# Performance work log

Hardware: AMD Instinct MI355X
Metric: run time of the kernel (lower is better)

## Reference

```python
import math
import jax, jax.numpy as jnp
import numpy as np

B, S, D, H = 2, 512, 1024, 8
DK = D // H
NSEP = 4


def setup_inputs() -> dict:
    key = jax.random.key(0)
    ks = jax.random.split(key, 16)
    inp = {
        'query': jax.random.normal(ks[0], (B, S, D), jnp.float32),
        'key': jax.random.normal(ks[1], (B, S, D), jnp.float32),
        'value': jax.random.normal(ks[2], (B, S, D), jnp.float32),
        'relation_k': jax.random.normal(ks[3], (B, S, S, DK), jnp.float32),
        'relation_v': jax.random.normal(ks[4], (B, S, S, DK), jnp.float32),
        'mask': jnp.ones((B, S, S), jnp.int32),
        'sep_id': jnp.sort(jax.random.randint(ks[5], (NSEP,), 0, S)),
        'history_reg': jax.random.uniform(ks[6], (1, NSEP), jnp.float32),
        'Wq': jax.random.normal(ks[7], (D, D), jnp.float32) / math.sqrt(D),
        'bq': jnp.zeros((D,), jnp.float32),
        'Wk': jax.random.normal(ks[8], (D, D), jnp.float32) / math.sqrt(D),
        'bk': jnp.zeros((D,), jnp.float32),
        'Wv': jax.random.normal(ks[9], (D, D), jnp.float32) / math.sqrt(D),
        'bv': jnp.zeros((D,), jnp.float32),
        'Wo': jax.random.normal(ks[10], (D, D), jnp.float32) / math.sqrt(D),
        'bo': jnp.zeros((D,), jnp.float32),
        'history_weights': jax.random.normal(ks[11], (H, DK), jnp.float32) / math.sqrt(DK),
    }
    return inp


def reference(query, key, value, relation_k, relation_v, mask, sep_id, history_reg,
              Wq, bq, Wk, bk, Wv, bv, Wo, bo, history_weights):
    b, s, d = query.shape
    h = history_weights.shape[0]
    dk = d // h
    scale = 1.0 / math.sqrt(dk)

    def proj(x, W, bb):
        return (x @ W.T + bb).reshape(b, s, h, dk).transpose(0, 2, 1, 3)  # [B,H,S,dk]

    q = proj(query, Wq, bq)
    k = proj(key, Wk, bk)
    v = proj(value, Wv, bv)

    # relation-aware logits: QK^T + Q.relation_k^T, scaled
    scores = (jnp.einsum('bhqd,bhkd->bhqk', q, k)
              + jnp.einsum('bhqd,bqkd->bhqk', q, relation_k)) * scale
    scores = jnp.where(mask[:, None, :, :] == 0, -1000000000.0, scores)

    # per-segment history reweighting
    sep_sel = q[:, :, sep_id, :]                                   # [B,H,n,dk]
    sep_pool = jnp.einsum('bhnd,hd->bhn', sep_sel, history_weights)
    sep_pred = jax.nn.softmax(sep_pool, axis=-1)                   # [B,H,n]

    pos = jnp.arange(s)
    ind = (pos[None, :] >= sep_id[:, None]).astype(scores.dtype)   # [n,S]
    g = jnp.einsum('bhn,np->bhp', sep_pred, ind)                   # cum weight per position
    minrc = jnp.minimum(pos[:, None], pos[None, :])                # [S,S]
    factor = g[:, :, minrc]                                        # [B,H,S,S]
    scores = scores * factor

    # losses
    loss = jnp.mean(1.0 - jnp.max(jnp.abs(sep_pred), axis=-1))
    log_pred = jnp.log(sep_pred).reshape(-1, sep_pred.shape[-1])
    tgt = jnp.broadcast_to(history_reg, log_pred.shape)
    loss = loss + jnp.mean(tgt * (jnp.log(tgt) - log_pred))

    p = jax.nn.softmax(scores, axis=-1)  # dropout is identity at eval
    x = (jnp.einsum('bhqk,bhkd->bhqd', p, v)
         + jnp.einsum('bhqk,bqkd->bhqd', p, relation_v))
    x = x.transpose(0, 2, 1, 3).reshape(b, s, d)
    out = x @ Wo.T + bo
    return out, loss
```

## Files before the change

### kernel.cpp

```cpp
#include <hip/hip_runtime.h>

static constexpr float SCALE = 0.08838834764831845f;

typedef __bf16 bf16;
typedef __bf16 bf16x8 __attribute__((ext_vector_type(8)));
typedef float  f32x4  __attribute__((ext_vector_type(4)));

#define MFMA16(a, b, c) __builtin_amdgcn_mfma_f32_16x16x32_bf16((a), (b), (c), 0, 0, 0)

__device__ inline bf16x8 cvt8(const float4& x, const float4& y) {
  bf16x8 r;
  r[0] = (bf16)x.x; r[1] = (bf16)x.y; r[2] = (bf16)x.z; r[3] = (bf16)x.w;
  r[4] = (bf16)y.x; r[5] = (bf16)y.y; r[6] = (bf16)y.z; r[7] = (bf16)y.w;
  return r;
}

__global__ __launch_bounds__(256)
void cvt_bf16(const float* __restrict__ s0, const float* __restrict__ s1,
              const float* __restrict__ s2, const float* __restrict__ s3,
              const float* __restrict__ s4, const float* __restrict__ s5,
              const float* __restrict__ s6,
              bf16* __restrict__ d0, bf16* __restrict__ d1,
              bf16* __restrict__ d2, bf16* __restrict__ d3,
              bf16* __restrict__ d4, bf16* __restrict__ d5,
              bf16* __restrict__ d6)
{
  const int sel = blockIdx.y;
  const float* src = sel == 0 ? s0 : sel == 1 ? s1 : sel == 2 ? s2 :
                     sel == 3 ? s3 : sel == 4 ? s4 : sel == 5 ? s5 : s6;
  bf16* dst = sel == 0 ? d0 : sel == 1 ? d1 : sel == 2 ? d2 :
              sel == 3 ? d3 : sel == 4 ? d4 : sel == 5 ? d5 : d6;
  const size_t idx = ((size_t)blockIdx.x * 256 + threadIdx.x) * 8;
  const float4 a = *(const float4*)(src + idx);
  const float4 b = *(const float4*)(src + idx + 4);
  *(bf16x8*)(dst + idx) = cvt8(a, b);
}

__global__ __launch_bounds__(256)
void proj3_mfma2(const bf16* __restrict__ Aq, const bf16* __restrict__ Ak,
                 const bf16* __restrict__ Av,
                 const bf16* __restrict__ Wq, const bf16* __restrict__ Wk,
                 const bf16* __restrict__ Wv,
                 const float* __restrict__ bq, const float* __restrict__ bk,
                 const float* __restrict__ bv,
                 float* __restrict__ qf, bf16* __restrict__ q16,
                 bf16* __restrict__ k16, bf16* __restrict__ vt16)
{
  const int sel = blockIdx.y;
  const bf16* A     = sel == 0 ? Aq : (sel == 1 ? Ak : Av);
  const bf16* W     = sel == 0 ? Wq : (sel == 1 ? Wk : Wv);
  const float* bias = sel == 0 ? bq : (sel == 1 ? bk : bv);

  __shared__ bf16 As[64][72];
  __shared__ bf16 Bs[64][72];
  const int t = threadIdx.x;
  const int m0 = (blockIdx.x >> 4) << 6;
  const int n0 = (blockIdx.x & 15) << 6;
  const int wave = t >> 6, lane = t & 63;
  const int wr = wave >> 1, wc = wave & 1;
  const int srow = t >> 2, skc = (t & 3) << 4;
  const bf16* Ap = A + (size_t)(m0 + srow) * 1024 + skc;
  const bf16* Wp = W + (size_t)(n0 + srow) * 1024 + skc;
  const int fr = lane & 15, kb = (lane >> 4) << 3;
  f32x4 acc[2][2];
#pragma unroll
  for (int i = 0; i < 2; ++i)
#pragma unroll
    for (int j = 0; j < 2; ++j) acc[i][j] = (f32x4){0.f, 0.f, 0.f, 0.f};

  uint4 a0 = *(const uint4*)Ap, a1 = *(const uint4*)(Ap + 8);
  uint4 b0 = *(const uint4*)Wp, b1 = *(const uint4*)(Wp + 8);
  uint4 a0n, a1n, b0n, b1n;
  for (int k0 = 0; k0 < 1024; k0 += 64) {
    __syncthreads();
    *(uint4*)&As[srow][skc]     = a0; *(uint4*)&As[srow][skc + 8] = a1;
    *(uint4*)&Bs[srow][skc]     = b0; *(uint4*)&Bs[srow][skc + 8] = b1;
    __syncthreads();
    if (k0 + 64 < 1024) {
      a0n = *(const uint4*)(Ap + k0 + 64); a1n = *(const uint4*)(Ap + k0 + 72);
      b0n = *(const uint4*)(Wp + k0 + 64); b1n = *(const uint4*)(Wp + k0 + 72);
    }
#pragma unroll
    for (int ks = 0; ks < 2; ++ks) {
      bf16x8 af[2], bff[2];
#pragma unroll
      for (int f = 0; f < 2; ++f) {
        af[f]  = *(const bf16x8*)&As[wr * 32 + f * 16 + fr][ks * 32 + kb];
        bff[f] = *(const bf16x8*)&Bs[wc * 32 + f * 16 + fr][ks * 32 + kb];
      }
#pragma unroll
      for (int i = 0; i < 2; ++i)
#pragma unroll
        for (int j = 0; j < 2; ++j)
          acc[i][j] = MFMA16(af[i], bff[j], acc[i][j]);
    }
    a0 = a0n; a1 = a1n; b0 = b0n; b1 = b1n;
  }
  const int lrow = (lane >> 4) << 2, lcol = lane & 15;
#pragma unroll
  for (int i = 0; i < 2; ++i) {
#pragma unroll
    for (int j = 0; j < 2; ++j) {
      const int n = n0 + wc * 32 + j * 16 + lcol;
      const float bvl = bias[n];
#pragma unroll
      for (int r = 0; r < 4; ++r) {
        const int m = m0 + wr * 32 + i * 16 + lrow + r;
        const float val = acc[i][j][r] + bvl;
        const int b = m >> 9, ii = m & 511, h = n >> 7, dk = n & 127;
        if (sel == 2) {
          vt16[(((size_t)(b * 8 + h) * 128) + dk) * 512 + ii] = (bf16)val;
        } else {
          const size_t idx = (((size_t)(b * 8 + h) * 512) + ii) * 128 + dk;
          if (sel == 0) { qf[idx] = val; q16[idx] = (bf16)val; }
          else          { k16[idx] = (bf16)val; }
        }
      }
    }
  }
}

__global__ __launch_bounds__(256)
void qs_fat(const bf16* __restrict__ Q, const bf16* __restrict__ Kb,
            float* __restrict__ scores,
            const float* __restrict__ qf, const float* __restrict__ hw,
            const int* __restrict__ sep_id, const float* __restrict__ hreg,
            float* __restrict__ g, float* __restrict__ loss_out)
{
  __shared__ bf16 As[64][72];
  __shared__ bf16 Bs[64][72];
  __shared__ float pool[16][4];
  __shared__ float spred[16][4];
  __shared__ float lbuf[16];
  __shared__ int sids[4];
  const int t = threadIdx.x;

  if (blockIdx.x >= 1024) {
    if (t < 4) sids[t] = sep_id[t];
    __syncthreads();
    {
      const int dot = t >> 2, sub = t & 3;
      const int bh = dot >> 2, n = dot & 3;
      const int b = bh >> 3, h = bh & 7;
      const int row = sids[n];
      const float* qp = qf + (((size_t)(b * 8 + h) * 512) + row) * 128 + sub * 32;
      const float* wp = hw + h * 128 + sub * 32;
      float s = 0.f;
#pragma unroll
      for (int dd = 0; dd < 32; ++dd) s = fmaf(qp[dd], wp[dd], s);
      s += __shfl_xor(s, 1);
      s += __shfl_xor(s, 2);
      if (sub == 0) pool[bh][n] = s;
    }
    __syncthreads();
    if (t < 16) {
      float pv[4];
#pragma unroll
      for (int n = 0; n < 4; ++n) pv[n] = pool[t][n];
      float mx = fmaxf(fmaxf(pv[0], pv[1]), fmaxf(pv[2], pv[3]));
      float sum = 0.f;
#pragma unroll
      for (int n = 0; n < 4; ++n) { pv[n] = expf(pv[n] - mx); sum += pv[n]; }
      const float inv = 1.f / sum;
      float maxp = 0.f, l2 = 0.f;
#pragma unroll
      for (int n = 0; n < 4; ++n) {
        const float pr = pv[n] * inv;
        spred[t][n] = pr;
        maxp = fmaxf(maxp, pr);
        const float tg = hreg[n];
        l2 += tg * (logf(tg) - logf(pr));
      }
      lbuf[t] = (1.f - maxp) / 16.f + l2 / 64.f;
    }
    __syncthreads();
    if (t == 0) {
      float L = 0.f;
#pragma unroll
      for (int r = 0; r < 16; ++r) L += lbuf[r];
      loss_out[0] = L;
    }
    for (int idx = t; idx < 16 * 512; idx += 256) {
      const int bh = idx >> 9, pp = idx & 511;
      float gg = 0.f;
#pragma unroll
      for (int n = 0; n < 4; ++n)
        gg += spred[bh][n] * (pp >= sids[n] ? 1.f : 0.f);
      g[idx] = gg;
    }
    return;
  }

  const int bh = blockIdx.x >> 6, tile = blockIdx.x & 63;
  const bf16* A = Q  + (size_t)bh * (512 * 128);
  const bf16* B = Kb + (size_t)bh * (512 * 128);
  float* C = scores + (size_t)bh * (512 * 512);
  const int m0 = (tile >> 3) << 6, n0 = (tile & 7) << 6;
  const int wave = t >> 6, lane = t & 63;
  const int wr = wave >> 1, wc = wave & 1;
  const int srow = t >> 2, skc = (t & 3) << 4;
  const int fr = lane & 15, kb = (lane >> 4) << 3;
  f32x4 acc[2][2];
#pragma unroll
  for (int i = 0; i < 2; ++i)
#pragma unroll
    for (int j = 0; j < 2; ++j) acc[i][j] = (f32x4){0.f, 0.f, 0.f, 0.f};

  const bf16* ap = A + (size_t)(m0 + srow) * 128 + skc;
  const bf16* bp = B + (size_t)(n0 + srow) * 128 + skc;
  uint4 a0 = *(const uint4*)ap, a1 = *(const uint4*)(ap + 8);
  uint4 b0 = *(const uint4*)bp, b1 = *(const uint4*)(bp + 8);
  for (int k0 = 0; k0 < 128; k0 += 64) {
    __syncthreads();
    *(uint4*)&As[srow][skc]     = a0; *(uint4*)&As[srow][skc + 8] = a1;
    *(uint4*)&Bs[srow][skc]     = b0; *(uint4*)&Bs[srow][skc + 8] = b1;
    __syncthreads();
    if (k0 == 0) {
      a0 = *(const uint4*)(ap + 64); a1 = *(const uint4*)(ap + 72);
      b0 = *(const uint4*)(bp + 64); b1 = *(const uint4*)(bp + 72);
    }
#pragma unroll
    for (int ks = 0; ks < 2; ++ks) {
      bf16x8 af[2], bff[2];
#pragma unroll
      for (int f = 0; f < 2; ++f) {
        af[f]  = *(const bf16x8*)&As[wr * 32 + f * 16 + fr][ks * 32 + kb];
        bff[f] = *(const bf16x8*)&Bs[wc * 32 + f * 16 + fr][ks * 32 + kb];
      }
#pragma unroll
      for (int i = 0; i < 2; ++i)
#pragma unroll
        for (int j = 0; j < 2; ++j)
          acc[i][j] = MFMA16(af[i], bff[j], acc[i][j]);
    }
  }
  const int lrow = (lane >> 4) << 2, lcol = lane & 15;
#pragma unroll
  for (int i = 0; i < 2; ++i)
#pragma unroll
    for (int j = 0; j < 2; ++j)
#pragma unroll
      for (int r = 0; r < 4; ++r) {
        const int m = m0 + wr * 32 + i * 16 + lrow + r;
        const int n = n0 + wc * 32 + j * 16 + lcol;
        C[(size_t)m * 512 + n] = acc[i][j][r];
      }
}

__global__ __launch_bounds__(256)
void relk_sm(const bf16* __restrict__ q16, const float* __restrict__ rk,
             const float* __restrict__ sc, const int* __restrict__ mask,
             const float* __restrict__ g, bf16* __restrict__ pb)
{
  const int bi = blockIdx.x, b = bi >> 9, i = bi & 511;
  __shared__ float rel_[8 * 516];
  const int t = threadIdx.x;
  const int w = t >> 6, lane = t & 63;
  const int fr = lane & 15, fg = lane >> 4;

  bf16x8 bq[4];
#pragma unroll
  for (int kt = 0; kt < 4; ++kt) {
    if (fr < 8) {
      bq[kt] = *(const bf16x8*)&q16[(((size_t)(b * 8 + fr) * 512) + i) * 128
                                    + kt * 32 + fg * 8];
    } else {
#pragma unroll
      for (int e = 0; e < 8; ++e) bq[kt][e] = (bf16)0.f;
    }
  }

  const float* rkb = rk + (size_t)bi * 512 * 128;
  for (int c = 0; c < 8; ++c) {
    const int jb = c * 64 + w * 16;
    const float* rp = rkb + (size_t)(jb + fr) * 128 + fg * 8;
    float4 a[8];
#pragma unroll
    for (int kt = 0; kt < 4; ++kt) {
      a[kt * 2]     = *(const float4*)(rp + kt * 32);
      a[kt * 2 + 1] = *(const float4*)(rp + kt * 32 + 4);
    }
    f32x4 acc = (f32x4){0.f, 0.f, 0.f, 0.f};
#pragma unroll
    for (int kt = 0; kt < 4; ++kt)
      acc = MFMA16(cvt8(a[kt * 2], a[kt * 2 + 1]), bq[kt], acc);
    if (fr < 8) {
#pragma unroll
      for (int r = 0; r < 4; ++r)
        rel_[fr * 516 + jb + fg * 4 + r] = acc[r];
    }
  }
  __syncthreads();

  const int h = t >> 5, ln = t & 31;
  const float* scrow = sc + (((size_t)(b * 8 + h) * 512) + i) * 512;
  const int* mrow = mask + ((size_t)(b * 512 + i)) * 512;
  const float* grow = g + (b * 8 + h) * 512;
  const float gi = grow[i];
  float s[16];
  float mx = -3.402823466e+38f;
#pragma unroll
  for (int k = 0; k < 16; ++k) {
    const int j = ln + (k << 5);
    float sv = (scrow[j] + rel_[h * 516 + j]) * SCALE;
    if (mrow[j] == 0) sv = -1.0e9f;
    const float fac = (j >= i) ? gi : grow[j];
    sv *= fac;
    s[k] = sv;
    mx = fmaxf(mx, sv);
  }
#pragma unroll
  for (int off = 16; off > 0; off >>= 1) mx = fmaxf(mx, __shfl_xor(mx, off));
  float sum = 0.f;
#pragma unroll
  for (int k = 0; k < 16; ++k) { const float e = __expf(s[k] - mx); s[k] = e; sum += e; }
#pragma unroll
  for (int off = 16; off > 0; off >>= 1) sum += __shfl_xor(sum, off);
  const float inv = 1.f / sum;
  bf16* prow = pb + (((size_t)(b * 8 + h) * 512) + i) * 512;
#pragma unroll
  for (int k = 0; k < 16; ++k) {
    const int j = ln + (k << 5);
    prow[j] = (bf16)(s[k] * inv);
  }
}

__global__ __launch_bounds__(256)
void relv_fat(const bf16* __restrict__ P, const bf16* __restrict__ VT,
              const float* __restrict__ rvg,
              float* __restrict__ xb2, float* __restrict__ xa)
{
  __shared__ __align__(16) char smem_raw[26032];
  const int t = threadIdx.x;

  if (blockIdx.x < 256) {
    bf16 (*As)[72] = (bf16(*)[72])&smem_raw[0];
    bf16 (*Bs)[72] = (bf16(*)[72])&smem_raw[9216];
    const int bh = blockIdx.x >> 4, tile = blockIdx.x & 15;
    const int b = bh >> 3, h = bh & 7;
    const bf16* A = P  + (size_t)bh * (512 * 512);
    const bf16* B = VT + (size_t)bh * (128 * 512);
    float* C = xb2 + (size_t)b * (512 * 1024) + h * 128;
    const int m0 = (tile >> 1) << 6, n0 = (tile & 1) << 6;
    const int wave = t >> 6, lane = t & 63;
    const int wr = wave >> 1, wc = wave & 1;
    const int srow = t >> 2, skc = (t & 3) << 4;
    const int fr = lane & 15, kb = (lane >> 4) << 3;
    f32x4 acc[2][2];
#pragma unroll
    for (int i = 0; i < 2; ++i)
#pragma unroll
      for (int j = 0; j < 2; ++j) acc[i][j] = (f32x4){0.f, 0.f, 0.f, 0.f};

    const bf16* ap = A + (size_t)(m0 + srow) * 512 + skc;
    const bf16* bp = B + (size_t)(n0 + srow) * 512 + skc;
    uint4 a0 = *(const uint4*)ap, a1 = *(const uint4*)(ap + 8);
    uint4 b0 = *(const uint4*)bp, b1 = *(const uint4*)(bp + 8);
    for (int k0 = 0; k0 < 512; k0 += 64) {
      __syncthreads();
      *(uint4*)&As[srow][skc]     = a0; *(uint4*)&As[srow][skc + 8] = a1;
      *(uint4*)&Bs[srow][skc]     = b0; *(uint4*)&Bs[srow][skc + 8] = b1;
      __syncthreads();
      if (k0 + 64 < 512) {
        a0 = *(const uint4*)(ap + k0 + 64); a1 = *(const uint4*)(ap + k0 + 72);
        b0 = *(const uint4*)(bp + k0 + 64); b1 = *(const uint4*)(bp + k0 + 72);
      }
#pragma unroll
      for (int ks = 0; ks < 2; ++ks) {
        bf16x8 af[2], bff[2];
#pragma unroll
        for (int f = 0; f < 2; ++f) {
          af[f]  = *(const bf16x8*)&As[wr * 32 + f * 16 + fr][ks * 32 + kb];
          bff[f] = *(const bf16x8*)&Bs[wc * 32 + f * 16 + fr][ks * 32 + kb];
        }
#pragma unroll
        for (int i = 0; i < 2; ++i)
#pragma unroll
          for (int j = 0; j < 2; ++j)
            acc[i][j] = MFMA16(af[i], bff[j], acc[i][j]);
      }
    }
    const int lrow = (lane >> 4) << 2, lcol = lane & 15;
#pragma unroll
    for (int i = 0; i < 2; ++i)
#pragma unroll
      for (int j = 0; j < 2; ++j)
#pragma unroll
        for (int r = 0; r < 4; ++r) {
          const int m = m0 + wr * 32 + i * 16 + lrow + r;
          const int n = n0 + wc * 32 + j * 16 + lcol;
          C[(size_t)m * 1024 + n] = acc[i][j][r];
        }
    return;
  }

  const int bi = blockIdx.x - 256, b = bi >> 9, i = bi & 511;
  bf16* p_lds = (bf16*)&smem_raw[0];
  bf16* rvT   = (bf16*)&smem_raw[9648];
  const int w = t >> 6, lane = t & 63;
  const int fr = lane & 15, fg = lane >> 4;

  {
    const int h = t >> 5, j0 = (t & 31) << 4;
    const bf16* src = P + (((size_t)(b * 8 + h) * 512) + i) * 512 + j0;
    const uint4 v0 = *(const uint4*)src;
    const uint4 v1 = *(const uint4*)(src + 8);
    *(uint4*)&p_lds[h * 536 + j0]     = v0;
    *(uint4*)&p_lds[h * 536 + j0 + 8] = v1;
  }

  const int arow = (fr < 8) ? fr : 8;
  const int ct0 = w * 2, ct1 = w * 2 + 1;
  f32x4 acc0 = (f32x4){0.f, 0.f, 0.f, 0.f};
  f32x4 acc1 = (f32x4){0.f, 0.f, 0.f, 0.f};

  for (int ch = 0; ch < 8; ++ch) {
    const int j0 = ch * 64;
    __syncthreads();
    {
      const int jj = t >> 5, d0 = (t & 31) << 2;
#pragma unroll
      for (int ps = 0; ps < 8; ++ps) {
        const int j = jj + ps * 8;
        const float4 rr = *(const float4*)&rvg[((size_t)bi * 512 + j0 + j) * 128 + d0];
        const float vr[4] = {rr.x, rr.y, rr.z, rr.w};
#pragma unroll
        for (int r = 0; r < 4; ++r) {
          const int d = d0 + r;
          const int blk = ((j >> 3) + (d >> 2)) & 7;
          rvT[d * 64 + blk * 8 + (j & 7)] = (bf16)vr[r];
        }
      }
    }
    __syncthreads();
#pragma unroll
    for (int kl = 0; kl < 2; ++kl) {
      const int jsub = kl * 32 + fg * 8;
      const bf16x8 af = *(const bf16x8*)&p_lds[arow * 536 + j0 + jsub];
      {
        const int d = ct0 * 16 + fr;
        const int blk = ((jsub >> 3) + (d >> 2)) & 7;
        const bf16x8 bf_ = *(const bf16x8*)&rvT[d * 64 + blk * 8];
        acc0 = MFMA16(af, bf_, acc0);
      }
      {
        const int d = ct1 * 16 + fr;
        const int blk = ((jsub >> 3) + (d >> 2)) & 7;
        const bf16x8 bf_ = *(const bf16x8*)&rvT[d * 64 + blk * 8];
        acc1 = MFMA16(af, bf_, acc1);
      }
    }
  }

  if (fg < 2) {
    float* xrow = xa + ((size_t)(b * 512 + i)) * 1024;
#pragma unroll
    for (int r = 0; r < 4; ++r) {
      const int h = fg * 4 + r;
      xrow[h * 128 + ct0 * 16 + fr] = acc0[r];
      xrow[h * 128 + ct1 * 16 + fr] = acc1[r];
    }
  }
}

__global__ __launch_bounds__(256)
void proj_out2(const float* __restrict__ A, const float* __restrict__ A2,
               const bf16* __restrict__ W16,
               const float* __restrict__ bias, float* __restrict__ Cf)
{
  __shared__ bf16 As[64][72];
  __shared__ bf16 Bs[64][72];
  const int t = threadIdx.x;
  const int m0 = (blockIdx.x >> 4) << 6;
  const int n0 = (blockIdx.x & 15) << 6;
  const int wave = t >> 6, lane = t & 63;
  const int wr = wave >> 1, wc = wave & 1;
  const int srow = t >> 2, skc = (t & 3) << 4;
  const float* Ap  = A   + (size_t)(m0 + srow) * 1024 + skc;
  const float* A2p = A2  + (size_t)(m0 + srow) * 1024 + skc;
  const bf16*  Wp  = W16 + (size_t)(n0 + srow) * 1024 + skc;
  const int fr = lane & 15, kb = (lane >> 4) << 3;
  f32x4 acc[2][2];
#pragma unroll
  for (int i = 0; i < 2; ++i)
#pragma unroll
    for (int j = 0; j < 2; ++j) acc[i][j] = (f32x4){0.f, 0.f, 0.f, 0.f};

  float4 a4[4], a4n[4];
  uint4 b0 = *(const uint4*)Wp, b1 = *(const uint4*)(Wp + 8);
  uint4 b0n, b1n;
#pragma unroll
  for (int u = 0; u < 4; ++u) {
    const float4 x1 = *(const float4*)(Ap + u * 4);
    const float4 x2 = *(const float4*)(A2p + u * 4);
    a4[u] = make_float4(x1.x + x2.x, x1.y + x2.y, x1.z + x2.z, x1.w + x2.w);
  }
  for (int k0 = 0; k0 < 1024; k0 += 64) {
    __syncthreads();
    *(bf16x8*)&As[srow][skc]     = cvt8(a4[0], a4[1]);
    *(bf16x8*)&As[srow][skc + 8] = cvt8(a4[2], a4[3]);
    *(uint4*)&Bs[srow][skc]      = b0;
    *(uint4*)&Bs[srow][skc + 8]  = b1;
    __syncthreads();
    if (k0 + 64 < 1024) {
#pragma unroll
      for (int u = 0; u < 4; ++u) {
        const float4 x1 = *(const float4*)(Ap + k0 + 64 + u * 4);
        const float4 x2 = *(const float4*)(A2p + k0 + 64 + u * 4);
        a4n[u] = make_float4(x1.x + x2.x, x1.y + x2.y, x1.z + x2.z, x1.w + x2.w);
      }
      b0n = *(const uint4*)(Wp + k0 + 64);
      b1n = *(const uint4*)(Wp + k0 + 72);
    }
#pragma unroll
    for (int ks = 0; ks < 2; ++ks) {
      bf16x8 af[2], bff[2];
#pragma unroll
      for (int f = 0; f < 2; ++f) {
        af[f]  = *(const bf16x8*)&As[wr * 32 + f * 16 + fr][ks * 32 + kb];
        bff[f] = *(const bf16x8*)&Bs[wc * 32 + f * 16 + fr][ks * 32 + kb];
      }
#pragma unroll
      for (int i = 0; i < 2; ++i)
#pragma unroll
        for (int j = 0; j < 2; ++j)
          acc[i][j] = MFMA16(af[i], bff[j], acc[i][j]);
    }
#pragma unroll
    for (int u = 0; u < 4; ++u) a4[u] = a4n[u];
    b0 = b0n; b1 = b1n;
  }
  const int lrow = (lane >> 4) << 2, lcol = lane & 15;
#pragma unroll
  for (int i = 0; i < 2; ++i) {
#pragma unroll
    for (int j = 0; j < 2; ++j) {
      const int n = n0 + wc * 32 + j * 16 + lcol;
      const float bvl = bias[n];
#pragma unroll
      for (int r = 0; r < 4; ++r) {
        const int m = m0 + wr * 32 + i * 16 + lrow + r;
        Cf[(size_t)m * 1024 + n] = acc[i][j][r] + bvl;
      }
    }
  }
}

extern "C" void kernel_launch(void* const* d_in, const int* in_sizes, int n_in,
                              void* d_out, int out_size, void* d_ws, size_t ws_size,
                              hipStream_t stream)
{
  const float* query = (const float*)d_in[0];
  const float* key   = (const float*)d_in[1];
  const float* value = (const float*)d_in[2];
  const float* rk    = (const float*)d_in[3];
  const float* rv    = (const float*)d_in[4];
  const int*   mask  = (const int*)d_in[5];
  const int*   sep   = (const int*)d_in[6];
  const float* hreg  = (const float*)d_in[7];
  const float* Wq    = (const float*)d_in[8];
  const float* bq    = (const float*)d_in[9];
  const float* Wk    = (const float*)d_in[10];
  const float* bk    = (const float*)d_in[11];
  const float* Wv    = (const float*)d_in[12];
  const float* bv    = (const float*)d_in[13];
  const float* Wo    = (const float*)d_in[14];
  const float* bo    = (const float*)d_in[15];
  const float* hw    = (const float*)d_in[16];
  float* out = (float*)d_out;

  float* ws  = (float*)d_ws;
  float* qb  = ws;
  float* sc  = qb + 1048576;
  float* xa  = sc + 4194304;
  float* xb2 = xa + 1048576;
  float* gb  = xb2 + 1048576;
  bf16* qb16 = (bf16*)(gb + 8192);
  bf16* kb16 = qb16 + 1048576;
  bf16* vt16 = kb16 + 1048576;
  bf16* pb16 = vt16 + 1048576;
  bf16* qA16 = pb16;
  bf16* kA16 = qA16 + 1048576;
  bf16* vA16 = kA16 + 1048576;
  bf16* Wq16 = vA16 + 1048576;
  bf16* Wk16 = pb16 + 4194304;
  bf16* Wv16 = Wk16 + 1048576;
  bf16* Wo16 = Wv16 + 1048576;

  cvt_bf16<<<dim3(512, 7), 256, 0, stream>>>(query, key, value, Wq, Wk, Wv, Wo,
                                             qA16, kA16, vA16, Wq16, Wk16, Wv16,
                                             Wo16);
  proj3_mfma2<<<dim3(256, 3), 256, 0, stream>>>(qA16, kA16, vA16,
                                                Wq16, Wk16, Wv16, bq, bk, bv,
                                                qb, qb16, kb16, vt16);
  qs_fat<<<dim3(1025), 256, 0, stream>>>(qb16, kb16, sc,
                                         qb, hw, sep, hreg, gb, out + 1048576);
  relk_sm<<<dim3(1024), 256, 0, stream>>>(qb16, rk, sc, mask, gb, pb16);
  relv_fat<<<dim3(1280), 256, 0, stream>>>(pb16, vt16, rv, xb2, xa);
  proj_out2<<<dim3(256), 256, 0, stream>>>(xa, xb2, Wo16, bo, out);
}
```

Measured before the change: 176.5 us.

## Double-buffer GEMM LDS tiles and stream relation_v directly from global into MFMA operands

The projection GEMMs now ping-pong between two LDS buffers, which removes one of the two barriers per k-step. The relation_v path in relv_fat no longer stages a transposed bf16 copy in LDS with a barrier per chunk. Instead each lane gathers strided fp32 values straight from global memory, converts them, and feeds them as the A operand with P as the B operand, which swaps the output layout. This drops LDS traffic and syncs, but the relation_v loads become scattered scalar reads that coalesce poorly and may raise global memory transactions.

```diff
diff --git a/kernel.cpp b/kernel.cpp
--- a/kernel.cpp
+++ b/kernel.cpp
@@ -51,8 +51,8 @@
   const bf16* W     = sel == 0 ? Wq : (sel == 1 ? Wk : Wv);
   const float* bias = sel == 0 ? bq : (sel == 1 ? bk : bv);
 
-  __shared__ bf16 As[64][72];
-  __shared__ bf16 Bs[64][72];
+  __shared__ bf16 As[2][64][72];
+  __shared__ bf16 Bs[2][64][72];
   const int t = threadIdx.x;
   const int m0 = (blockIdx.x >> 4) << 6;
   const int n0 = (blockIdx.x & 15) << 6;
@@ -72,21 +72,21 @@
   uint4 b0 = *(const uint4*)Wp, b1 = *(const uint4*)(Wp + 8);
   uint4 a0n, a1n, b0n, b1n;
   for (int k0 = 0; k0 < 1024; k0 += 64) {
-    __syncthreads();
-    *(uint4*)&As[srow][skc]     = a0; *(uint4*)&As[srow][skc + 8] = a1;
-    *(uint4*)&Bs[srow][skc]     = b0; *(uint4*)&Bs[srow][skc + 8] = b1;
-    __syncthreads();
+    const int buf = (k0 >> 6) & 1;
+    *(uint4*)&As[buf][srow][skc]     = a0; *(uint4*)&As[buf][srow][skc + 8] = a1;
+    *(uint4*)&Bs[buf][srow][skc]     = b0; *(uint4*)&Bs[buf][srow][skc + 8] = b1;
     if (k0 + 64 < 1024) {
       a0n = *(const uint4*)(Ap + k0 + 64); a1n = *(const uint4*)(Ap + k0 + 72);
       b0n = *(const uint4*)(Wp + k0 + 64); b1n = *(const uint4*)(Wp + k0 + 72);
     }
+    __syncthreads();
 #pragma unroll
     for (int ks = 0; ks < 2; ++ks) {
       bf16x8 af[2], bff[2];
 #pragma unroll
       for (int f = 0; f < 2; ++f) {
-        af[f]  = *(const bf16x8*)&As[wr * 32 + f * 16 + fr][ks * 32 + kb];
-        bff[f] = *(const bf16x8*)&Bs[wc * 32 + f * 16 + fr][ks * 32 + kb];
+        af[f]  = *(const bf16x8*)&As[buf][wr * 32 + f * 16 + fr][ks * 32 + kb];
+        bff[f] = *(const bf16x8*)&Bs[buf][wc * 32 + f * 16 + fr][ks * 32 + kb];
       }
 #pragma unroll
       for (int i = 0; i < 2; ++i)
@@ -330,7 +330,7 @@
               const float* __restrict__ rvg,
               float* __restrict__ xb2, float* __restrict__ xa)
 {
-  __shared__ __align__(16) char smem_raw[26032];
+  __shared__ __align__(16) char smem_raw[18432];
   const int t = threadIdx.x;
 
   if (blockIdx.x < 256) {
@@ -396,7 +396,6 @@
 
   const int bi = blockIdx.x - 256, b = bi >> 9, i = bi & 511;
   bf16* p_lds = (bf16*)&smem_raw[0];
-  bf16* rvT   = (bf16*)&smem_raw[9648];
   const int w = t >> 6, lane = t & 63;
   const int fr = lane & 15, fg = lane >> 4;
 
@@ -408,57 +407,36 @@
     *(uint4*)&p_lds[h * 536 + j0]     = v0;
     *(uint4*)&p_lds[h * 536 + j0 + 8] = v1;
   }
-
-  const int arow = (fr < 8) ? fr : 8;
+  __syncthreads();
+
   const int ct0 = w * 2, ct1 = w * 2 + 1;
   f32x4 acc0 = (f32x4){0.f, 0.f, 0.f, 0.f};
   f32x4 acc1 = (f32x4){0.f, 0.f, 0.f, 0.f};
-
-  for (int ch = 0; ch < 8; ++ch) {
-    const int j0 = ch * 64;
-    __syncthreads();
-    {
-      const int jj = t >> 5, d0 = (t & 31) << 2;
-#pragma unroll
-      for (int ps = 0; ps < 8; ++ps) {
-        const int j = jj + ps * 8;
-        const float4 rr = *(const float4*)&rvg[((size_t)bi * 512 + j0 + j) * 128 + d0];
-        const float vr[4] = {rr.x, rr.y, rr.z, rr.w};
-#pragma unroll
-        for (int r = 0; r < 4; ++r) {
-          const int d = d0 + r;
-          const int blk = ((j >> 3) + (d >> 2)) & 7;
-          rvT[d * 64 + blk * 8 + (j & 7)] = (bf16)vr[r];
-        }
-      }
-    }
-    __syncthreads();
-#pragma unroll
-    for (int kl = 0; kl < 2; ++kl) {
-      const int jsub = kl * 32 + fg * 8;
-      const bf16x8 af = *(const bf16x8*)&p_lds[arow * 536 + j0 + jsub];
-      {
-        const int d = ct0 * 16 + fr;
-        const int blk = ((jsub >> 3) + (d >> 2)) & 7;
-        const bf16x8 bf_ = *(const bf16x8*)&rvT[d * 64 + blk * 8];
-        acc0 = MFMA16(af, bf_, acc0);
-      }
-      {
-        const int d = ct1 * 16 + fr;
-        const int blk = ((jsub >> 3) + (d >> 2)) & 7;
-        const bf16x8 bf_ = *(const bf16x8*)&rvT[d * 64 + blk * 8];
-        acc1 = MFMA16(af, bf_, acc1);
-      }
-    }
-  }
-
-  if (fg < 2) {
-    float* xrow = xa + ((size_t)(b * 512 + i)) * 1024;
+  const float* rvb = rvg + (size_t)bi * 512 * 128;
+
+  for (int js = 0; js < 16; ++js) {
+    const int jb = js * 32 + fg * 8;
+    const bf16x8 bp = *(const bf16x8*)&p_lds[(fr & 7) * 536 + jb];
+    float a0v[8], a1v[8];
+#pragma unroll
+    for (int e = 0; e < 8; ++e) {
+      const float* col = rvb + (size_t)(jb + e) * 128 + fr;
+      a0v[e] = col[ct0 * 16];
+      a1v[e] = col[ct1 * 16];
+    }
+    bf16x8 af0, af1;
+#pragma unroll
+    for (int e = 0; e < 8; ++e) { af0[e] = (bf16)a0v[e]; af1[e] = (bf16)a1v[e]; }
+    acc0 = MFMA16(af0, bp, acc0);
+    acc1 = MFMA16(af1, bp, acc1);
+  }
+
+  if (fr < 8) {
+    float* xrow = xa + ((size_t)(b * 512 + i)) * 1024 + fr * 128;
 #pragma unroll
     for (int r = 0; r < 4; ++r) {
-      const int h = fg * 4 + r;
-      xrow[h * 128 + ct0 * 16 + fr] = acc0[r];
-      xrow[h * 128 + ct1 * 16 + fr] = acc1[r];
+      xrow[ct0 * 16 + fg * 4 + r] = acc0[r];
+      xrow[ct1 * 16 + fg * 4 + r] = acc1[r];
     }
   }
 }
@@ -468,8 +446,8 @@
                const bf16* __restrict__ W16,
                const float* __restrict__ bias, float* __restrict__ Cf)
 {
-  __shared__ bf16 As[64][72];
-  __shared__ bf16 Bs[64][72];
+  __shared__ bf16 As[2][64][72];
+  __shared__ bf16 Bs[2][64][72];
   const int t = threadIdx.x;
   const int m0 = (blockIdx.x >> 4) << 6;
   const int n0 = (blockIdx.x & 15) << 6;
@@ -496,12 +474,11 @@
     a4[u] = make_float4(x1.x + x2.x, x1.y + x2.y, x1.z + x2.z, x1.w + x2.w);
   }
   for (int k0 = 0; k0 < 1024; k0 += 64) {
-    __syncthreads();
-    *(bf16x8*)&As[srow][skc]     = cvt8(a4[0], a4[1]);
-    *(bf16x8*)&As[srow][skc + 8] = cvt8(a4[2], a4[3]);
-    *(uint4*)&Bs[srow][skc]      = b0;
-    *(uint4*)&Bs[srow][skc + 8]  = b1;
-    __syncthreads();
+    const int buf = (k0 >> 6) & 1;
+    *(bf16x8*)&As[buf][srow][skc]     = cvt8(a4[0], a4[1]);
+    *(bf16x8*)&As[buf][srow][skc + 8] = cvt8(a4[2], a4[3]);
+    *(uint4*)&Bs[buf][srow][skc]      = b0;
+    *(uint4*)&Bs[buf][srow][skc + 8]  = b1;
     if (k0 + 64 < 1024) {
 #pragma unroll
       for (int u = 0; u < 4; ++u) {
@@ -512,13 +489,14 @@
       b0n = *(const uint4*)(Wp + k0 + 64);
       b1n = *(const uint4*)(Wp + k0 + 72);
     }
+    __syncthreads();
 #pragma unroll
     for (int ks = 0; ks < 2; ++ks) {
       bf16x8 af[2], bff[2];
 #pragma unroll
       for (int f = 0; f < 2; ++f) {
-        af[f]  = *(const bf16x8*)&As[wr * 32 + f * 16 + fr][ks * 32 + kb];
-        bff[f] = *(const bf16x8*)&Bs[wc * 32 + f * 16 + fr][ks * 32 + kb];
+        af[f]  = *(const bf16x8*)&As[buf][wr * 32 + f * 16 + fr][ks * 32 + kb];
+        bff[f] = *(const bf16x8*)&Bs[buf][wc * 32 + f * 16 + fr][ks * 32 + kb];
       }
 #pragma unroll
       for (int i = 0; i < 2; ++i)
```

Result: no change. 174.8 us (-1.0%).
